# Performance work log

Measured on AMD Instinct MI355X. Metric: run time of the kernel, lower is better.

## Reference

```python
import jax, jax.numpy as jnp
import numpy as np

B, N, D = 1, 2048, 1024
L, H, DH = 4, 16, 64
INNER = H * DH            # 1024, == D
FF = int(D * 4.0)         # 4096 (GEGLU inner)
SCALE = DH ** -0.5
LN_EPS = 1e-5


def setup_inputs() -> dict:
    key = jax.random.key(0)
    ks = jax.random.split(key, 8)
    w = 0.02
    inp = {
        'x': jax.random.normal(ks[0], (B, N, D), jnp.float32),
        'mask': jnp.ones((B, N), dtype=bool),
        # stacked per-layer params (leading dim L)
        'Wqkv': jax.random.normal(ks[1], (L, D, 3 * INNER), jnp.float32) * w,
        'Wo': jax.random.normal(ks[2], (L, INNER, D), jnp.float32) * w,
        'bo': jnp.zeros((L, D), jnp.float32),
        'ln1_g': jnp.ones((L, D), jnp.float32),
        'ln1_b': jnp.zeros((L, D), jnp.float32),
        'ln2_g': jnp.ones((L, D), jnp.float32),
        'ln2_b': jnp.zeros((L, D), jnp.float32),
        'ls1': jnp.full((L, D), 0.1, jnp.float32),  # LayerScale init_eps=0.1 (depth<=18)
        'ls2': jnp.full((L, D), 0.1, jnp.float32),
        'W1': jax.random.normal(ks[3], (L, D, 2 * FF), jnp.float32) * w,
        'b1': jnp.zeros((L, 2 * FF), jnp.float32),
        'W2': jax.random.normal(ks[4], (L, FF, D), jnp.float32) * w,
        'b2': jnp.zeros((L, D), jnp.float32),
    }
    return inp


def _layernorm(x, g, b):
    mu = jnp.mean(x, axis=-1, keepdims=True)
    var = jnp.mean(jnp.square(x - mu), axis=-1, keepdims=True)
    return (x - mu) * jax.lax.rsqrt(var + LN_EPS) * g + b


def _forward(x, mask, Wqkv, Wo, bo, ln1_g, ln1_b, ln2_g, ln2_b, ls1, ls2, W1, b1, W2, b2):
    n = x.shape[1]
    causal = jnp.arange(n)[None, :] > jnp.arange(n)[:, None]  # True = masked
    valid = mask[:, None, None, :] & ~causal[None, None]       # (B,1,N,N) True = keep
    for l in range(L):
        # --- attention sublayer: x + LayerScale(PreNorm(Attn))(x) ---
        h = _layernorm(x, ln1_g[l], ln1_b[l])
        qkv = h @ Wqkv[l]                                      # (B,N,3*INNER)
        q, k, v = jnp.split(qkv, 3, axis=-1)
        q = q.reshape(B, n, H, DH).transpose(0, 2, 1, 3) * SCALE
        k = k.reshape(B, n, H, DH).transpose(0, 2, 1, 3)
        v = v.reshape(B, n, H, DH).transpose(0, 2, 1, 3)
        dots = jnp.einsum('bhid,bhjd->bhij', q, k)             # (B,H,N,N)
        neg = -jnp.finfo(dots.dtype).max
        dots = jnp.where(valid, dots, neg)
        attn = jax.nn.softmax(dots, axis=-1)                   # stable_softmax, temp=1
        o = jnp.einsum('bhij,bhjd->bhid', attn, v)
        o = o.transpose(0, 2, 1, 3).reshape(B, n, INNER)
        o = o @ Wo[l] + bo[l]
        x = x + o * ls1[l]
        # --- feedforward sublayer: x + LayerScale(PreNorm(GEGLU-FFN))(x) ---
        h = _layernorm(x, ln2_g[l], ln2_b[l])
        u = h @ W1[l] + b1[l]                                  # (B,N,2*FF)
        a, g = jnp.split(u, 2, axis=-1)
        f = (a * jax.nn.gelu(g, approximate=False)) @ W2[l] + b2[l]
        x = x + f * ls2[l]
    return x


def reference(x, mask, Wqkv, Wo, bo, ln1_g, ln1_b, ln2_g, ln2_b, ls1, ls2, W1, b1, W2, b2):
    return _forward(x, mask, Wqkv, Wo, bo, ln1_g, ln1_b, ln2_g, ln2_b, ls1, ls2, W1, b1, W2, b2)
```

## Files before the change

kernel.cpp:

```cpp
#include <hip/hip_runtime.h>
#include <hip/hip_bf16.h>
#include <math.h>

#define LN_EPS 1e-5f
#define ATT_SCALE 0.125f

typedef __bf16 bf16x8 __attribute__((ext_vector_type(8)));
typedef float f32x4 __attribute__((ext_vector_type(4)));

__device__ __forceinline__ unsigned short f2bf(float f){
  unsigned int u = __builtin_bit_cast(unsigned int, f);
  u += 0x7fffu + ((u >> 16) & 1u);
  return (unsigned short)(u >> 16);
}
__device__ __forceinline__ float bfbits2f(unsigned int lo16){
  return __builtin_bit_cast(float, lo16 << 16);
}

__global__ __launch_bounds__(256) void ln_kernel(
    const float* __restrict__ X, const float* __restrict__ g,
    const float* __restrict__ b, unsigned short* __restrict__ H)
{
  __shared__ float red[4];
  int row = blockIdx.x, t = threadIdx.x;
  const float4 xv = ((const float4*)(X + (size_t)row*1024))[t];
  float s = xv.x + xv.y + xv.z + xv.w;
  #pragma unroll
  for (int o=32;o;o>>=1) s += __shfl_down(s,o);
  if ((t&63)==0) red[t>>6] = s;
  __syncthreads();
  float mu = (red[0]+red[1]+red[2]+red[3]) * (1.f/1024.f);
  __syncthreads();
  float dx = xv.x-mu, dy = xv.y-mu, dz = xv.z-mu, dw = xv.w-mu;
  float s2 = dx*dx+dy*dy+dz*dz+dw*dw;
  #pragma unroll
  for (int o=32;o;o>>=1) s2 += __shfl_down(s2,o);
  if ((t&63)==0) red[t>>6] = s2;
  __syncthreads();
  float var = (red[0]+red[1]+red[2]+red[3]) * (1.f/1024.f);
  float rs = rsqrtf(var + LN_EPS);
  const float4 gv = ((const float4*)g)[t];
  const float4 bv = ((const float4*)b)[t];
  ushort4 o4;
  o4.x = f2bf(dx*rs*gv.x + bv.x);
  o4.y = f2bf(dy*rs*gv.y + bv.y);
  o4.z = f2bf(dz*rs*gv.z + bv.z);
  o4.w = f2bf(dw*rs*gv.w + bv.w);
  ((ushort4*)(H + (size_t)row*1024))[t] = o4;
}

template<int SK, int DO_LN>
__global__ __launch_bounds__(256) void redln_kernel(
    const unsigned short* __restrict__ P, float* __restrict__ X,
    const float* __restrict__ bias, const float* __restrict__ scale,
    const float* __restrict__ g, const float* __restrict__ b,
    unsigned short* __restrict__ H)
{
  __shared__ float red[4];
  int row = blockIdx.x, t = threadIdx.x;
  size_t off = (size_t)row*1024 + t*4;
  float4 xv = *(const float4*)(X + off);
  float4 pv;
  {
    uint2 u = *(const uint2*)(P + off);
    pv.x = bfbits2f(u.x & 0xffffu); pv.y = bfbits2f(u.x >> 16);
    pv.z = bfbits2f(u.y & 0xffffu); pv.w = bfbits2f(u.y >> 16);
  }
  #pragma unroll
  for (int c=1;c<SK;c++){
    uint2 u = *(const uint2*)(P + (size_t)c*2048*1024 + off);
    pv.x += bfbits2f(u.x & 0xffffu); pv.y += bfbits2f(u.x >> 16);
    pv.z += bfbits2f(u.y & 0xffffu); pv.w += bfbits2f(u.y >> 16);
  }
  const float4 bv = ((const float4*)bias)[t];
  const float4 sv = ((const float4*)scale)[t];
  xv.x += (pv.x+bv.x)*sv.x;
  xv.y += (pv.y+bv.y)*sv.y;
  xv.z += (pv.z+bv.z)*sv.z;
  xv.w += (pv.w+bv.w)*sv.w;
  *(float4*)(X + off) = xv;
  if (DO_LN){
    float s = xv.x + xv.y + xv.z + xv.w;
    #pragma unroll
    for (int o=32;o;o>>=1) s += __shfl_down(s,o);
    if ((t&63)==0) red[t>>6] = s;
    __syncthreads();
    float mu = (red[0]+red[1]+red[2]+red[3]) * (1.f/1024.f);
    __syncthreads();
    float dx = xv.x-mu, dy = xv.y-mu, dz = xv.z-mu, dw = xv.w-mu;
    float s2 = dx*dx+dy*dy+dz*dz+dw*dw;
    #pragma unroll
    for (int o=32;o;o>>=1) s2 += __shfl_down(s2,o);
    if ((t&63)==0) red[t>>6] = s2;
    __syncthreads();
    float var = (red[0]+red[1]+red[2]+red[3]) * (1.f/1024.f);
    float rs = rsqrtf(var + LN_EPS);
    const float4 gv = ((const float4*)g)[t];
    const float4 lbv = ((const float4*)b)[t];
    ushort4 o4;
    o4.x = f2bf(dx*rs*gv.x + lbv.x);
    o4.y = f2bf(dy*rs*gv.y + lbv.y);
    o4.z = f2bf(dz*rs*gv.z + lbv.z);
    o4.w = f2bf(dw*rs*gv.w + lbv.w);
    ((ushort4*)(H + (size_t)row*1024))[t] = o4;
  }
}

__global__ __launch_bounds__(256) void trc_kernel(
    const float* __restrict__ W, unsigned short* __restrict__ WT, int K, int N)
{
  __shared__ float tile[64][65];
  const float* Wz = W + (size_t)blockIdx.z*K*N;
  unsigned short* WTz = WT + (size_t)blockIdx.z*K*N;
  int n0 = blockIdx.x*64, k0 = blockIdx.y*64;
  int t = threadIdx.x;
  int tx = t & 63, ty = t >> 6;
  #pragma unroll
  for (int p=0;p<16;p++){
    int r = ty*16+p;
    tile[r][tx] = Wz[(size_t)(k0+r)*N + n0 + tx];
  }
  __syncthreads();
  int kc = t & 31, tb = t >> 5;
  #pragma unroll
  for (int p=0;p<8;p++){
    int nr = tb + p*8;
    unsigned int lo = f2bf(tile[2*kc][nr]);
    unsigned int hi = f2bf(tile[2*kc+1][nr]);
    ((unsigned int*)(WTz + (size_t)(n0+nr)*K + k0))[kc] = lo | (hi<<16);
  }
}

__global__ __launch_bounds__(256) void trc_w1_kernel(
    const float* __restrict__ W, unsigned short* __restrict__ WT)
{
  __shared__ float tile[64][65];
  const float* Wz = W + (size_t)blockIdx.z*1024*8192;
  unsigned short* WTz = WT + (size_t)blockIdx.z*1024*8192;
  int n0 = blockIdx.x*64, k0 = blockIdx.y*64;
  int ca = (n0>>5)*16;
  int t = threadIdx.x;
  int tx = t & 63, ty = t >> 6;
  #pragma unroll
  for (int p=0;p<16;p++){
    int r = ty*16+p;
    int col = (tx < 32) ? (ca + tx) : (ca + 4064 + tx);
    tile[r][tx] = Wz[(size_t)(k0+r)*8192 + col];
  }
  __syncthreads();
  int kc = t & 31, tb = t >> 5;
  #pragma unroll
  for (int p=0;p<8;p++){
    int nr = tb + p*8;
    int rr = nr & 31;
    int vcol = (nr>>5)*16 + (rr&15) + ((rr>>4)<<5);
    unsigned int lo = f2bf(tile[2*kc][vcol]);
    unsigned int hi = f2bf(tile[2*kc+1][vcol]);
    ((unsigned int*)(WTz + (size_t)(n0+nr)*1024 + k0))[kc] = lo | (hi<<16);
  }
}

template<int MODE, int SWZ>
__global__ __launch_bounds__(256) void gemm_bt(
    const unsigned short* __restrict__ A, const unsigned short* __restrict__ BT,
    int M, int N, int K,
    unsigned short* __restrict__ Obf,
    const float* __restrict__ bias)
{
  __shared__ unsigned short Asm[2][128*64];
  __shared__ unsigned short Bsm[2][128*64];
  int t = threadIdx.x;
  int lane = t & 63;
  int w = t >> 6, wm = w >> 1, wn = w & 1;

  int bn, bm;
  if (SWZ){
    int nwg = gridDim.x * gridDim.y;
    int wg = blockIdx.y * gridDim.x + blockIdx.x;
    int cpx = nwg >> 3;
    int swz = (wg & 7) * cpx + (wg >> 3);
    bn = swz % gridDim.x; bm = swz / gridDim.x;
  } else {
    bn = blockIdx.x; bm = blockIdx.y;
  }

  f32x4 acc[4][4] = {};
  int ktBeg = 0, ktEnd = K >> 6;
  if (MODE == 3){
    int per = (K >> 6) / gridDim.z;
    ktBeg = blockIdx.z * per;
    ktEnd = ktBeg + per;
  }

  int srow = t >> 3, ssc = t & 7;
  auto STAGE = [&](int kt, int buf){
    #pragma unroll
    for (int c=0;c<4;c++){
      int row = c*32 + srow;
      int gc = ssc ^ (row & 7);
      const unsigned short* sa = A  + (size_t)(bm*128 + row)*K + kt*64 + gc*8;
      const unsigned short* sb = BT + (size_t)(bn*128 + row)*K + kt*64 + gc*8;
      __builtin_amdgcn_global_load_lds(
        (const __attribute__((address_space(1))) unsigned int*)sa,
        (__attribute__((address_space(3))) unsigned int*)(&Asm[buf][(c*256 + (t & ~63))*8]),
        16, 0, 0);
      __builtin_amdgcn_global_load_lds(
        (const __attribute__((address_space(1))) unsigned int*)sb,
        (__attribute__((address_space(3))) unsigned int*)(&Bsm[buf][(c*256 + (t & ~63))*8]),
        16, 0, 0);
    }
  };

  STAGE(ktBeg, 0);
  __syncthreads();
  int cur = 0;
  for (int kt = ktBeg; kt < ktEnd; ++kt){
    if (kt + 1 < ktEnd) STAGE(kt + 1, cur ^ 1);
    #pragma unroll
    for (int kk=0;kk<2;kk++){
      bf16x8 aF[4], bF[4];
      #pragma unroll
      for (int m=0;m<4;m++){
        int row = wm*64 + m*16 + (lane&15);
        int ch = kk*4 + (lane>>4);
        aF[m] = *(const bf16x8*)&Asm[cur][row*64 + (ch ^ (row&7))*8];
      }
      #pragma unroll
      for (int n=0;n<4;n++){
        int row = wn*64 + n*16 + (lane&15);
        int ch = kk*4 + (lane>>4);
        bF[n] = *(const bf16x8*)&Bsm[cur][row*64 + (ch ^ (row&7))*8];
      }
      __builtin_amdgcn_s_setprio(1);
      #pragma unroll
      for (int m=0;m<4;m++)
        #pragma unroll
        for (int n=0;n<4;n++)
          acc[m][n] = __builtin_amdgcn_mfma_f32_16x16x32_bf16(aF[m], bF[n], acc[m][n], 0,0,0);
      __builtin_amdgcn_s_setprio(0);
    }
    __syncthreads();
    cur ^= 1;
  }

  unsigned short* ep = &Asm[0][0];
  int colg = lane & 15;
  int r0 = wm*64 + (lane>>4)*4;
  if (MODE==4){
    float b1a[2], b1g[2];
    #pragma unroll
    for (int p=0;p<2;p++){
      int oc = (bn*4 + wn*2 + p)*16 + colg;
      b1a[p] = bias[oc];
      b1g[p] = bias[oc + 4096];
    }
    #pragma unroll
    for (int m=0;m<4;m++){
      #pragma unroll
      for (int p=0;p<2;p++){
        int cw = (wn*2 + p)*16 + colg;
        #pragma unroll
        for (int j=0;j<4;j++){
          float va = acc[m][2*p][j]   + b1a[p];
          float vg = acc[m][2*p+1][j] + b1g[p];
          float f = va * (0.5f * vg * (1.f + erff(vg * 0.70710678118f)));
          ep[(r0 + m*16 + j)*64 + cw] = f2bf(f);
        }
      }
    }
    __syncthreads();
    #pragma unroll
    for (int i=0;i<4;i++){
      int idx = i*256 + t;
      int row = idx >> 3, ch = idx & 7;
      *(uint4*)&Obf[(size_t)(bm*128+row)*4096 + bn*64 + ch*8] = *(const uint4*)&ep[row*64 + ch*8];
    }
    return;
  }
  #pragma unroll
  for (int m=0;m<4;m++)
    #pragma unroll
    for (int n=0;n<4;n++){
      int cw = wn*64 + n*16 + colg;
      #pragma unroll
      for (int j=0;j<4;j++)
        ep[(r0 + m*16 + j)*128 + cw] = f2bf(acc[m][n][j]);
    }
  __syncthreads();
  size_t zoff = (MODE==3) ? (size_t)blockIdx.z*((size_t)M*N) : 0;
  #pragma unroll
  for (int i=0;i<8;i++){
    int idx = i*256 + t;
    int row = idx >> 4, ch = idx & 15;
    *(uint4*)&Obf[zoff + (size_t)(bm*128+row)*N + bn*128 + ch*8] = *(const uint4*)&ep[row*128 + ch*8];
  }
}

__global__ __launch_bounds__(256) void vtr_kernel(
    const unsigned short* __restrict__ qkv, unsigned short* __restrict__ VT)
{
  __shared__ unsigned int tile[64][33];
  int h = blockIdx.y;
  int n0 = blockIdx.x * 64;
  int t = threadIdx.x;
  #pragma unroll
  for (int p=0;p<8;p++){
    int idx = p*256 + t;
    int r = idx >> 5, c = idx & 31;
    tile[r][c] = *(const unsigned int*)(qkv + (size_t)(n0+r)*3072 + 2048 + h*64 + c*2);
  }
  __syncthreads();
  #pragma unroll
  for (int p=0;p<8;p++){
    int idx = p*256 + t;
    int d = idx >> 5, c = idx & 31;
    unsigned int a = tile[2*c][d>>1];
    unsigned int b = tile[2*c+1][d>>1];
    unsigned int lo = (d&1) ? (a>>16) : (a & 0xffffu);
    unsigned int hi = (d&1) ? (b>>16) : (b & 0xffffu);
    *(unsigned int*)(VT + (size_t)h*131072 + (size_t)d*2048 + n0 + c*2) = lo | (hi<<16);
  }
}

__global__ __launch_bounds__(256) void flash_attn(
    const unsigned short* __restrict__ qkv,
    const unsigned short* __restrict__ VT,
    unsigned short* __restrict__ O)
{
  __shared__ unsigned short Klds[2][64*64];
  __shared__ unsigned short Vlds[2][64*64];
  __shared__ unsigned short Plds[4][16*72];
  __shared__ float fbuf[4][16];
  __shared__ float lbuf[4][16];

  int t = threadIdx.x;
  int lane = t & 63;
  int w = t >> 6;
  int q15 = lane & 15, l16 = lane >> 4;

  int bid = blockIdx.x;
  int x = bid & 7, r = bid >> 3;
  int h = 2*x + (r & 1);
  int q = r >> 1;
  int qt = (q < 16) ? q : 47 - q;
  int q0 = qt * 64;

  bf16x8 qF[2];
  int qrow = q0 + w*16 + q15;
  #pragma unroll
  for (int db=0; db<2; db++)
    qF[db] = *(const bf16x8*)(qkv + (size_t)qrow*3072 + h*64 + db*32 + l16*8);

  int srow = t >> 3, ssc = t & 7;
  auto STAGE = [&](int kt, int buf){
    int k0 = kt*64;
    #pragma unroll
    for (int c=0;c<2;c++){
      int row = c*32 + srow;
      int gc = ssc ^ (row & 7);
      const unsigned short* sk = qkv + (size_t)(k0+row)*3072 + 1024 + h*64 + gc*8;
      const unsigned short* sv = VT + (size_t)h*131072 + (size_t)row*2048 + k0 + gc*8;
      __builtin_amdgcn_global_load_lds(
        (const __attribute__((address_space(1))) unsigned int*)sk,
        (__attribute__((address_space(3))) unsigned int*)(&Klds[buf][(c*256 + (t & ~63))*8]),
        16, 0, 0);
      __builtin_amdgcn_global_load_lds(
        (const __attribute__((address_space(1))) unsigned int*)sv,
        (__attribute__((address_space(3))) unsigned int*)(&Vlds[buf][(c*256 + (t & ~63))*8]),
        16, 0, 0);
    }
  };

  f32x4 o[4] = {};
  float m_run = -1e30f, l_run = 0.f;

  STAGE(0, 0);
  __syncthreads();
  int cur = 0;
  for (int kt = 0; kt <= qt; ++kt){
    if (kt < qt) STAGE(kt + 1, cur ^ 1);

    f32x4 s[4] = {};
    #pragma unroll
    for (int km=0;km<4;km++){
      #pragma unroll
      for (int db=0;db<2;db++){
        int row = km*16 + q15;
        int ch = db*4 + l16;
        bf16x8 kF = *(const bf16x8*)&Klds[cur][row*64 + (ch ^ (row&7))*8];
        s[km] = __builtin_amdgcn_mfma_f32_16x16x32_bf16(kF, qF[db], s[km], 0,0,0);
      }
    }

    bool diag = (kt == qt);
    float pmax = -1e30f;
    #pragma unroll
    for (int km=0;km<4;km++){
      #pragma unroll
      for (int j=0;j<4;j++){
        float sv = s[km][j] * ATT_SCALE;
        if (diag){
          int kg = km*16 + l16*4 + j;
          int qg = w*16 + q15;
          if (kg > qg) sv = -1e30f;
        }
        s[km][j] = sv;
        pmax = fmaxf(pmax, sv);
      }
    }
    pmax = fmaxf(pmax, __shfl_xor(pmax, 16));
    pmax = fmaxf(pmax, __shfl_xor(pmax, 32));

    float m_new = fmaxf(m_run, pmax);
    float f = __expf(m_run - m_new);

    float lsum = 0.f;
    #pragma unroll
    for (int km=0;km<4;km++){
      float p0 = __expf(s[km][0]-m_new);
      float p1 = __expf(s[km][1]-m_new);
      float p2 = __expf(s[km][2]-m_new);
      float p3 = __expf(s[km][3]-m_new);
      lsum += (p0+p1)+(p2+p3);
      unsigned int v0 = (unsigned int)f2bf(p0) | ((unsigned int)f2bf(p1)<<16);
      unsigned int v1 = (unsigned int)f2bf(p2) | ((unsigned int)f2bf(p3)<<16);
      *(uint2*)&Plds[w][q15*72 + km*16 + l16*4] = make_uint2(v0,v1);
    }
    lsum += __shfl_xor(lsum,16);
    lsum += __shfl_xor(lsum,32);
    l_run = l_run * f + lsum;
    m_run = m_new;

    if (l16 == 0) fbuf[w][q15] = f;
    f32x4 fv = *(f32x4*)&fbuf[w][l16*4];
    #pragma unroll
    for (int n=0;n<4;n++) o[n] *= fv;

    #pragma unroll
    for (int kb=0;kb<2;kb++){
      bf16x8 aP = *(const bf16x8*)&Plds[w][q15*72 + kb*32 + l16*8];
      #pragma unroll
      for (int n=0;n<4;n++){
        int row = n*16 + q15;
        int ch = kb*4 + l16;
        bf16x8 vF = *(const bf16x8*)&Vlds[cur][row*64 + (ch ^ (row&7))*8];
        o[n] = __builtin_amdgcn_mfma_f32_16x16x32_bf16(aP, vF, o[n], 0,0,0);
      }
    }
    __syncthreads();
    cur ^= 1;
  }

  if (l16 == 0) lbuf[w][q15] = 1.f / l_run;
  f32x4 lv = *(f32x4*)&lbuf[w][l16*4];

  #pragma unroll
  for (int n=0;n<4;n++){
    #pragma unroll
    for (int j=0;j<4;j++){
      int row = q0 + w*16 + l16*4 + j;
      int col = h*64 + n*16 + q15;
      O[(size_t)row*1024 + col] = f2bf(o[n][j]*lv[j]);
    }
  }
}

extern "C" void kernel_launch(void* const* d_in, const int* in_sizes, int n_in,
                              void* d_out, int out_size, void* d_ws, size_t ws_size,
                              hipStream_t stream)
{
  (void)in_sizes; (void)n_in; (void)out_size; (void)ws_size;
  const float* x_in = (const float*)d_in[0];
  const float* Wqkv = (const float*)d_in[2];
  const float* Wo   = (const float*)d_in[3];
  const float* bo   = (const float*)d_in[4];
  const float* ln1g = (const float*)d_in[5];
  const float* ln1b = (const float*)d_in[6];
  const float* ln2g = (const float*)d_in[7];
  const float* ln2b = (const float*)d_in[8];
  const float* ls1  = (const float*)d_in[9];
  const float* ls2  = (const float*)d_in[10];
  const float* W1   = (const float*)d_in[11];
  const float* b1   = (const float*)d_in[12];
  const float* W2   = (const float*)d_in[13];
  const float* b2   = (const float*)d_in[14];
  float* X = (float*)d_out;

  char* ws = (char*)d_ws;
  unsigned short* WTq = (unsigned short*)(ws);
  unsigned short* WTo = (unsigned short*)(ws + (24u<<20));
  unsigned short* WT1 = (unsigned short*)(ws + (32u<<20));
  unsigned short* WT2 = (unsigned short*)(ws + (96u<<20));
  unsigned short* hb  = (unsigned short*)(ws + (128u<<20));
  unsigned short* qu  = (unsigned short*)(ws + (132u<<20));
  unsigned short* VTg = (unsigned short*)(ws + (144u<<20));
  unsigned short* of  = (unsigned short*)(ws + (148u<<20));
  unsigned short* PTb = (unsigned short*)(ws + (164u<<20));

  hipMemcpyAsync(d_out, (const void*)x_in, (size_t)2048*1024*4,
                 hipMemcpyDeviceToDevice, stream);

  trc_kernel<<<dim3(3072/64,1024/64,4),256,0,stream>>>(Wqkv, WTq, 1024, 3072);
  trc_kernel<<<dim3(1024/64,1024/64,4),256,0,stream>>>(Wo,   WTo, 1024, 1024);
  trc_w1_kernel<<<dim3(8192/64,1024/64,4),256,0,stream>>>(W1, WT1);
  trc_kernel<<<dim3(1024/64,4096/64,4),256,0,stream>>>(W2,   WT2, 4096, 1024);

  for (int l = 0; l < 4; ++l){
    if (l == 0)
      ln_kernel<<<2048,256,0,stream>>>(X, ln1g, ln1b, hb);
    gemm_bt<0,0><<<dim3(3072/128,2048/128),256,0,stream>>>(hb, WTq + (size_t)l*3072*1024,
        2048,3072,1024, qu, nullptr);
    vtr_kernel<<<dim3(32,16),256,0,stream>>>(qu, VTg);
    flash_attn<<<512,256,0,stream>>>(qu, VTg, of);
    gemm_bt<3,1><<<dim3(1024/128,2048/128,2),256,0,stream>>>(of, WTo + (size_t)l*1024*1024,
        2048,1024,1024, PTb, nullptr);
    redln_kernel<2,1><<<2048,256,0,stream>>>(PTb, X, bo + l*1024, ls1 + l*1024,
        ln2g + l*1024, ln2b + l*1024, hb);
    gemm_bt<4,0><<<dim3(8192/128,2048/128),256,0,stream>>>(hb, WT1 + (size_t)l*8192*1024,
        2048,8192,1024, of, b1 + (size_t)l*8192);
    gemm_bt<3,1><<<dim3(1024/128,2048/128,4),256,0,stream>>>(of, WT2 + (size_t)l*1024*4096,
        2048,1024,4096, PTb, nullptr);
    if (l < 3)
      redln_kernel<4,1><<<2048,256,0,stream>>>(PTb, X, b2 + l*1024, ls2 + l*1024,
          ln1g + (l+1)*1024, ln1b + (l+1)*1024, hb);
    else
      redln_kernel<4,0><<<2048,256,0,stream>>>(PTb, X, b2 + l*1024, ls2 + l*1024,
          nullptr, nullptr, nullptr);
  }
}
```

Before: 796.6 us.

## Load K/V fragments directly from global and skip softmax rescale lazily

The flash attention kernel no longer stages K and V tiles into double-buffered LDS with async global-to-LDS loads and block barriers. Each wave now reads its MFMA K and V fragments straight from global memory, relying on cache reuse across the four waves. It also adds a lazy online-softmax rescale that only updates the running max and rescales the accumulators when the new max exceeds the old one by more than 8. This trades barrier and LDS overhead for redundant global/L2 traffic, and exposes load latency without explicit prefetch.

```diff
diff --git a/kernel.cpp b/kernel.cpp
--- a/kernel.cpp
+++ b/kernel.cpp
@@ -327,8 +327,6 @@
     const unsigned short* __restrict__ VT,
     unsigned short* __restrict__ O)
 {
-  __shared__ unsigned short Klds[2][64*64];
-  __shared__ unsigned short Vlds[2][64*64];
   __shared__ unsigned short Plds[4][16*72];
   __shared__ float fbuf[4][16];
   __shared__ float lbuf[4][16];
@@ -351,43 +349,21 @@
   for (int db=0; db<2; db++)
     qF[db] = *(const bf16x8*)(qkv + (size_t)qrow*3072 + h*64 + db*32 + l16*8);
 
-  int srow = t >> 3, ssc = t & 7;
-  auto STAGE = [&](int kt, int buf){
-    int k0 = kt*64;
-    #pragma unroll
-    for (int c=0;c<2;c++){
-      int row = c*32 + srow;
-      int gc = ssc ^ (row & 7);
-      const unsigned short* sk = qkv + (size_t)(k0+row)*3072 + 1024 + h*64 + gc*8;
-      const unsigned short* sv = VT + (size_t)h*131072 + (size_t)row*2048 + k0 + gc*8;
-      __builtin_amdgcn_global_load_lds(
-        (const __attribute__((address_space(1))) unsigned int*)sk,
-        (__attribute__((address_space(3))) unsigned int*)(&Klds[buf][(c*256 + (t & ~63))*8]),
-        16, 0, 0);
-      __builtin_amdgcn_global_load_lds(
-        (const __attribute__((address_space(1))) unsigned int*)sv,
-        (__attribute__((address_space(3))) unsigned int*)(&Vlds[buf][(c*256 + (t & ~63))*8]),
-        16, 0, 0);
-    }
-  };
+  const unsigned short* Kb = qkv + 1024 + h*64;
+  const unsigned short* Vb = VT + (size_t)h*131072;
 
   f32x4 o[4] = {};
   float m_run = -1e30f, l_run = 0.f;
 
-  STAGE(0, 0);
-  __syncthreads();
-  int cur = 0;
   for (int kt = 0; kt <= qt; ++kt){
-    if (kt < qt) STAGE(kt + 1, cur ^ 1);
+    int k0 = kt*64;
 
     f32x4 s[4] = {};
     #pragma unroll
     for (int km=0;km<4;km++){
       #pragma unroll
       for (int db=0;db<2;db++){
-        int row = km*16 + q15;
-        int ch = db*4 + l16;
-        bf16x8 kF = *(const bf16x8*)&Klds[cur][row*64 + (ch ^ (row&7))*8];
+        bf16x8 kF = *(const bf16x8*)(Kb + (size_t)(k0 + km*16 + q15)*3072 + db*32 + l16*8);
         s[km] = __builtin_amdgcn_mfma_f32_16x16x32_bf16(kF, qF[db], s[km], 0,0,0);
       }
     }
@@ -411,16 +387,24 @@
     pmax = fmaxf(pmax, __shfl_xor(pmax, 16));
     pmax = fmaxf(pmax, __shfl_xor(pmax, 32));
 
-    float m_new = fmaxf(m_run, pmax);
-    float f = __expf(m_run - m_new);
+    if (!__all(pmax - m_run <= 8.f)){
+      float m_new = fmaxf(m_run, pmax);
+      float f = __expf(m_run - m_new);
+      m_run = m_new;
+      l_run *= f;
+      if (l16 == 0) fbuf[w][q15] = f;
+      f32x4 fv = *(f32x4*)&fbuf[w][l16*4];
+      #pragma unroll
+      for (int n=0;n<4;n++) o[n] *= fv;
+    }
 
     float lsum = 0.f;
     #pragma unroll
     for (int km=0;km<4;km++){
-      float p0 = __expf(s[km][0]-m_new);
-      float p1 = __expf(s[km][1]-m_new);
-      float p2 = __expf(s[km][2]-m_new);
-      float p3 = __expf(s[km][3]-m_new);
+      float p0 = __expf(s[km][0]-m_run);
+      float p1 = __expf(s[km][1]-m_run);
+      float p2 = __expf(s[km][2]-m_run);
+      float p3 = __expf(s[km][3]-m_run);
       lsum += (p0+p1)+(p2+p3);
       unsigned int v0 = (unsigned int)f2bf(p0) | ((unsigned int)f2bf(p1)<<16);
       unsigned int v1 = (unsigned int)f2bf(p2) | ((unsigned int)f2bf(p3)<<16);
@@ -428,27 +412,17 @@
     }
     lsum += __shfl_xor(lsum,16);
     lsum += __shfl_xor(lsum,32);
-    l_run = l_run * f + lsum;
-    m_run = m_new;
-
-    if (l16 == 0) fbuf[w][q15] = f;
-    f32x4 fv = *(f32x4*)&fbuf[w][l16*4];
-    #pragma unroll
-    for (int n=0;n<4;n++) o[n] *= fv;
+    l_run += lsum;
 
     #pragma unroll
     for (int kb=0;kb<2;kb++){
       bf16x8 aP = *(const bf16x8*)&Plds[w][q15*72 + kb*32 + l16*8];
       #pragma unroll
       for (int n=0;n<4;n++){
-        int row = n*16 + q15;
-        int ch = kb*4 + l16;
-        bf16x8 vF = *(const bf16x8*)&Vlds[cur][row*64 + (ch ^ (row&7))*8];
+        bf16x8 vF = *(const bf16x8*)(Vb + (size_t)(n*16 + q15)*2048 + k0 + kb*32 + l16*8);
         o[n] = __builtin_amdgcn_mfma_f32_16x16x32_bf16(aP, vF, o[n], 0,0,0);
       }
     }
-    __syncthreads();
-    cur ^= 1;
   }
 
   if (l16 == 0) lbuf[w][q15] = 1.f / l_run;
```

Measured after the change: 904.6 us. 1.14x slower.
